# Performance work log

Measured on AMD Instinct MI355X. Metric: run time of the kernel, lower is better.

## Reference

```python
import jax, jax.numpy as jnp
import numpy as np

BITS = 4
SPLIT_BITS = 4  # `ratio` arg plays the role of split_bits in the torch Function


def _chunk_quant(src, bits):
    """src: [n_chunks, chunk_elems...]; quantize each chunk with its own min/max."""
    reduce_axes = tuple(range(1, src.ndim))
    mn = src.min(axis=reduce_axes, keepdims=True)
    mx = src.max(axis=reduce_axes, keepdims=True)
    levels = jnp.asarray(2 ** bits - 1, src.dtype)
    step = (mx - mn) / levels
    safe_step = jnp.where(step == 0, jnp.ones_like(step), step)
    # torch: round((s-min)/step) - 2^(b-1); then (+2^(b-1))*step + min  ==  round(...)*step + min
    q = jnp.round((src - mn) / safe_step) * safe_step + mn
    # if min == max the chunk is passed through unchanged
    return jnp.where(mn == mx, src, q)


def setup_inputs() -> dict:
    key = jax.random.key(0)
    x = jax.random.normal(key, (16, 2048, 2048), dtype=jnp.float32)
    return {"x": x}


def reference(x) -> jnp.ndarray:
    shape = x.shape
    flat = x.reshape(-1)
    n_chunks = 2 ** SPLIT_BITS  # 16; flat.size divisible by 16 by construction
    order = jnp.argsort(flat)            # ascending sort permutation
    src = flat[order].reshape(n_chunks, -1)
    q = _chunk_quant(src, BITS).reshape(-1)
    # scatter quantized values back to original positions: out[order[i]] = q[i]
    inv = jnp.argsort(order)
    out = q[inv]
    return out.reshape(shape)
```

## Files before the change

### kernel.cpp

```cpp
#include <hip/hip_runtime.h>
#include <math.h>

#define L1BITS 14
#define L1B 16384
#define L1W (L1B / 2)
#define H1_BLOCKS 512
#define SLOTS 32
#define L2BITS 9
#define L2B 512
#define L3BITS 9
#define L3B 512
#define H2_BLOCKS 256
#define H2W (SLOTS * L2B / 2)

__device__ unsigned int g_part1[H1_BLOCKS * L1W];
__device__ unsigned int g_part2[H2_BLOCKS * H2W];
__device__ unsigned int g_hist1[L1B];
__device__ unsigned int g_coarse1[L1B / 256];
__device__ unsigned int g_hist2[SLOTS * L2B];
__device__ unsigned int g_hist3[SLOTS * L3B];
__device__ unsigned char g_sid1[L1B];
__device__ unsigned char g_sid2[SLOTS * L2B];

__device__ unsigned int g_bin1[32], g_res1[32];
__device__ int          g_slot1[32];
__device__ unsigned int g_bin2[32], g_res2[32];
__device__ int          g_slot2[32];
__device__ float        g_mn[16], g_mx[16];
__device__ unsigned int g_tkey[16];

__device__ __forceinline__ unsigned int f2key(float f) {
    unsigned int b = __float_as_uint(f);
    return (b & 0x80000000u) ? ~b : (b | 0x80000000u);
}
__device__ __forceinline__ float key2f(unsigned int k) {
    unsigned int b = (k & 0x80000000u) ? (k & 0x7FFFFFFFu) : ~k;
    return __uint_as_float(b);
}

__global__ void zero_scratch() {
    int i = blockIdx.x * blockDim.x + threadIdx.x;
    int stride = gridDim.x * blockDim.x;
    for (int j = i; j < L1B; j += stride) g_hist1[j] = 0u;
    for (int j = i; j < SLOTS * L2B; j += stride) g_hist2[j] = 0u;
    for (int j = i; j < SLOTS * L3B; j += stride) g_hist3[j] = 0u;
    unsigned int* s1 = (unsigned int*)g_sid1;
    for (int j = i; j < L1B / 4; j += stride) s1[j] = 0u;
    unsigned int* s2 = (unsigned int*)g_sid2;
    for (int j = i; j < SLOTS * L2B / 4; j += stride) s2[j] = 0u;
    if (i < L1B / 256) g_coarse1[i] = 0u;
}

__global__ void hist1_kernel(const float4* __restrict__ x, int n4) {
    __shared__ unsigned int h[2 * L1W];
    for (int j = threadIdx.x; j < 2 * L1W; j += blockDim.x) h[j] = 0u;
    __syncthreads();
    unsigned int* hp = &h[((threadIdx.x >> 6) & 1) * L1W];
    int stride = gridDim.x * blockDim.x;
    for (int i = blockIdx.x * blockDim.x + threadIdx.x; i < n4; i += stride) {
        float4 v = x[i];
        float vv[4] = {v.x, v.y, v.z, v.w};
#pragma unroll
        for (int k = 0; k < 4; ++k) {
            unsigned int b = f2key(vv[k]) >> (32 - L1BITS);
            atomicAdd(&hp[b >> 1], 1u << ((b & 1) << 4));
        }
    }
    __syncthreads();
    for (int j = threadIdx.x; j < L1W; j += blockDim.x) {
        unsigned int a = h[j], b = h[L1W + j];
        unsigned int lo = (a & 0xFFFFu) + (b & 0xFFFFu);
        unsigned int hi = (a >> 16) + (b >> 16);
        g_part1[blockIdx.x * L1W + j] = lo | (hi << 16);
    }
}

__global__ void reduce1_kernel() {
    int t = blockIdx.x * blockDim.x + threadIdx.x;
    int w = t & (L1W - 1);
    int chunk = t >> 13;
    const unsigned int* p = &g_part1[(chunk * 64) * L1W + w];
    unsigned int lo = 0, hi = 0;
#pragma unroll 8
    for (int b = 0; b < 64; ++b) {
        unsigned int u = p[b * L1W];
        lo += u & 0xFFFFu;
        hi += u >> 16;
    }
    atomicAdd(&g_hist1[2 * w], lo);
    atomicAdd(&g_hist1[2 * w + 1], hi);
    unsigned int s = lo + hi;
#pragma unroll
    for (int off = 32; off; off >>= 1) s += (unsigned int)__shfl_down((int)s, off, 64);
    if ((threadIdx.x & 63) == 0) atomicAdd(&g_coarse1[w >> 7], s);
}

__device__ __forceinline__ void wave_select(const unsigned int* __restrict__ hist,
                                            int nbins, unsigned int r,
                                            unsigned int* out_bin, unsigned int* out_res) {
    int lane = threadIdx.x & 63;
    unsigned int base = 0;
    for (int k = 0; k < nbins; k += 64) {
        unsigned int v = hist[k + lane];
        unsigned int incl = v;
#pragma unroll
        for (int off = 1; off < 64; off <<= 1) {
            unsigned int t = (unsigned int)__shfl_up((int)incl, off, 64);
            if (lane >= off) incl += t;
        }
        unsigned int total = (unsigned int)__shfl((int)incl, 63, 64);
        if (r < base + total) {
            unsigned long long m = __ballot(base + incl > r);
            int fl = __ffsll((long long)m) - 1;
            unsigned int incl_fl = (unsigned int)__shfl((int)incl, fl, 64);
            unsigned int v_fl = (unsigned int)__shfl((int)v, fl, 64);
            *out_bin = (unsigned int)(k + fl);
            *out_res = r - (base + incl_fl - v_fl);
            return;
        }
        base += total;
    }
    *out_bin = (unsigned int)(nbins - 1);
    *out_res = 0;
}

__global__ void select1_kernel(unsigned int n) {
    __shared__ unsigned int s_bin[32], s_res[32];
    int wid = threadIdx.x >> 6;
    unsigned int M = n >> 4;
    for (int i = wid; i < 32; i += 16) {
        unsigned int c = (unsigned int)(i >> 1);
        unsigned int r = (i & 1) ? ((c + 1) * M - 1u) : (c * M);
        unsigned int g, rg, b, res;
        wave_select(g_coarse1, L1B / 256, r, &g, &rg);
        wave_select(g_hist1 + (g << 8), 256, rg, &b, &res);
        if ((threadIdx.x & 63) == 0) { s_bin[i] = (g << 8) | b; s_res[i] = res; }
    }
    __syncthreads();
    if (threadIdx.x == 0) {
        int nu = 0;
        for (int i = 0; i < 32; ++i) {
            unsigned int b = s_bin[i];
            if (g_sid1[b] == 0) g_sid1[b] = (unsigned char)(++nu);
            g_slot1[i] = g_sid1[b] - 1;
            g_bin1[i] = b;
            g_res1[i] = s_res[i];
        }
    }
}

__global__ void hist2_kernel(const float4* __restrict__ x, int n4) {
    __shared__ unsigned int h2[H2W];
    __shared__ unsigned char sid1[L1B];
    for (int j = threadIdx.x; j < H2W; j += blockDim.x) h2[j] = 0u;
    unsigned int* s1w = (unsigned int*)sid1;
    for (int j = threadIdx.x; j < L1B / 4; j += blockDim.x) s1w[j] = ((const unsigned int*)g_sid1)[j];
    __syncthreads();
    int stride = gridDim.x * blockDim.x;
    for (int i = blockIdx.x * blockDim.x + threadIdx.x; i < n4; i += stride) {
        float4 v = x[i];
        float vv[4] = {v.x, v.y, v.z, v.w};
#pragma unroll
        for (int k = 0; k < 4; ++k) {
            unsigned int key = f2key(vv[k]);
            unsigned int s = sid1[key >> (32 - L1BITS)];
            if (s) {
                unsigned int c = ((s - 1) << L2BITS) | ((key >> L3BITS) & (L2B - 1));
                atomicAdd(&h2[c >> 1], 1u << ((c & 1) << 4));
            }
        }
    }
    __syncthreads();
    for (int j = threadIdx.x; j < H2W; j += blockDim.x)
        g_part2[blockIdx.x * H2W + j] = h2[j];
}

__global__ void reduce2_kernel() {
    int t = blockIdx.x * blockDim.x + threadIdx.x;
    int w = t & (H2W - 1);
    int chunk = t >> 13;
    const unsigned int* p = &g_part2[(chunk * 32) * H2W + w];
    unsigned int lo = 0, hi = 0;
#pragma unroll 8
    for (int b = 0; b < 32; ++b) {
        unsigned int u = p[b * H2W];
        lo += u & 0xFFFFu;
        hi += u >> 16;
    }
    atomicAdd(&g_hist2[2 * w], lo);
    atomicAdd(&g_hist2[2 * w + 1], hi);
}

__global__ void select2_kernel() {
    __shared__ unsigned int s_bin[32], s_res[32];
    int wid = threadIdx.x >> 6;
    for (int i = wid; i < 32; i += 16) {
        int s = g_slot1[i];
        unsigned int b, res;
        wave_select(g_hist2 + (s << L2BITS), L2B, g_res1[i], &b, &res);
        if ((threadIdx.x & 63) == 0) { s_bin[i] = b; s_res[i] = res; }
    }
    __syncthreads();
    if (threadIdx.x == 0) {
        int nu = 0;
        for (int i = 0; i < 32; ++i) {
            int p = g_slot1[i] * L2B + (int)s_bin[i];
            if (g_sid2[p] == 0) g_sid2[p] = (unsigned char)(++nu);
            g_slot2[i] = g_sid2[p] - 1;
            g_bin2[i] = s_bin[i];
            g_res2[i] = s_res[i];
        }
    }
}

__global__ void hist3_kernel(const float4* __restrict__ x, int n4) {
    __shared__ unsigned char sid1[L1B];
    __shared__ unsigned char sid2[SLOTS * L2B];
    unsigned int* s1w = (unsigned int*)sid1;
    for (int j = threadIdx.x; j < L1B / 4; j += blockDim.x) s1w[j] = ((const unsigned int*)g_sid1)[j];
    unsigned int* s2w = (unsigned int*)sid2;
    for (int j = threadIdx.x; j < SLOTS * L2B / 4; j += blockDim.x) s2w[j] = ((const unsigned int*)g_sid2)[j];
    __syncthreads();
    int stride = gridDim.x * blockDim.x;
    for (int i = blockIdx.x * blockDim.x + threadIdx.x; i < n4; i += stride) {
        float4 v = x[i];
        float vv[4] = {v.x, v.y, v.z, v.w};
#pragma unroll
        for (int k = 0; k < 4; ++k) {
            unsigned int key = f2key(vv[k]);
            unsigned int s = sid1[key >> (32 - L1BITS)];
            if (s) {
                unsigned int s2 = sid2[((s - 1) << L2BITS) | ((key >> L3BITS) & (L2B - 1))];
                if (s2) atomicAdd(&g_hist3[((s2 - 1) << L3BITS) | (key & (L3B - 1))], 1u);
            }
        }
    }
}

__global__ void select3_kernel() {
    __shared__ unsigned int s_key[32];
    int wid = threadIdx.x >> 6;
    for (int i = wid; i < 32; i += 16) {
        int s2 = g_slot2[i];
        unsigned int b, res;
        wave_select(g_hist3 + (s2 << L3BITS), L3B, g_res2[i], &b, &res);
        if ((threadIdx.x & 63) == 0)
            s_key[i] = (g_bin1[i] << (32 - L1BITS)) | (g_bin2[i] << L3BITS) | b;
    }
    __syncthreads();
    if (threadIdx.x < 16) {
        int c = threadIdx.x;
        unsigned int klo = s_key[2 * c];
        unsigned int khi = s_key[2 * c + 1];
        g_mn[c] = key2f(klo);
        g_mx[c] = key2f(khi);
        g_tkey[c] = (c == 0) ? 0u : klo;
    }
}

__global__ void quant_kernel(const float4* __restrict__ x, float4* __restrict__ out, int n4) {
    __shared__ float s_mn[16], s_mx[16];
    __shared__ unsigned int s_t[16];
    if (threadIdx.x < 16) {
        s_mn[threadIdx.x] = g_mn[threadIdx.x];
        s_mx[threadIdx.x] = g_mx[threadIdx.x];
        s_t[threadIdx.x]  = g_tkey[threadIdx.x];
    }
    __syncthreads();
    int stride = gridDim.x * blockDim.x;
    for (int i = blockIdx.x * blockDim.x + threadIdx.x; i < n4; i += stride) {
        float4 v = x[i];
        float r[4] = {v.x, v.y, v.z, v.w};
#pragma unroll
        for (int k = 0; k < 4; ++k) {
            float xv = r[k];
            unsigned int key = f2key(xv);
            int c = (key >= s_t[8]) ? 8 : 0;
            if (key >= s_t[c + 4]) c += 4;
            if (key >= s_t[c + 2]) c += 2;
            if (key >= s_t[c + 1]) c += 1;
            float mn = s_mn[c], mx = s_mx[c];
            float outv;
            if (mn == mx) {
                outv = xv;
            } else {
                float st = (mx - mn) / 15.0f;
                if (st == 0.0f) st = 1.0f;
                float q = rintf((xv - mn) / st);
                outv = __fadd_rn(__fmul_rn(q, st), mn);
            }
            r[k] = outv;
        }
        out[i] = make_float4(r[0], r[1], r[2], r[3]);
    }
}

extern "C" void kernel_launch(void* const* d_in, const int* in_sizes, int n_in,
                              void* d_out, int out_size, void* d_ws, size_t ws_size,
                              hipStream_t stream) {
    const float* x = (const float*)d_in[0];
    float* out = (float*)d_out;
    int n  = in_sizes[0];
    int n4 = n / 4;

    zero_scratch<<<64, 256, 0, stream>>>();
    hist1_kernel<<<H1_BLOCKS, 512, 0, stream>>>((const float4*)x, n4);
    reduce1_kernel<<<256, 256, 0, stream>>>();
    select1_kernel<<<1, 1024, 0, stream>>>((unsigned int)n);
    hist2_kernel<<<H2_BLOCKS, 512, 0, stream>>>((const float4*)x, n4);
    reduce2_kernel<<<256, 256, 0, stream>>>();
    select2_kernel<<<1, 1024, 0, stream>>>();
    hist3_kernel<<<1024, 512, 0, stream>>>((const float4*)x, n4);
    select3_kernel<<<1, 1024, 0, stream>>>();
    quant_kernel<<<4096, 256, 0, stream>>>((const float4*)x, (float4*)out, n4);
}
```

Baseline: 707.2 us.

## Compact candidate keys during level-2 pass to skip third full input scan

The level-2 histogram pass now also writes the keys that fall in selected level-1 bins into per-block segments, and the level-3 histogram reads only those compacted keys instead of rescanning the whole input. This removes one full read of the 256 MB tensor and the separate reduce2 kernel, since level-2 partials are atomically merged straight into the global histogram. Zeroing of scratch moves into hist1, hist1 drops its duplicated shared histogram and runs with larger blocks, and the loops are unrolled to batch loads. The cost is extra global writes for candidate keys, wave-level ballot/atomic overhead, and a fixed segment size that silently truncates if too many keys are selected.

```diff
diff --git a/kernel.cpp b/kernel.cpp
--- a/kernel.cpp
+++ b/kernel.cpp
@@ -10,11 +10,13 @@
 #define L2B 512
 #define L3BITS 9
 #define L3B 512
-#define H2_BLOCKS 256
 #define H2W (SLOTS * L2B / 2)
+#define CBLK 256
+#define SEGSZ 262144
 
 __device__ unsigned int g_part1[H1_BLOCKS * L1W];
-__device__ unsigned int g_part2[H2_BLOCKS * H2W];
+__device__ unsigned int g_keys[CBLK * SEGSZ];
+__device__ unsigned int g_kcnt[CBLK];
 __device__ unsigned int g_hist1[L1B];
 __device__ unsigned int g_coarse1[L1B / 256];
 __device__ unsigned int g_hist2[SLOTS * L2B];
@@ -38,41 +40,42 @@
     return __uint_as_float(b);
 }
 
-__global__ void zero_scratch() {
-    int i = blockIdx.x * blockDim.x + threadIdx.x;
+__global__ void hist1_kernel(const float4* __restrict__ x, int n4) {
+    int gtid = blockIdx.x * blockDim.x + threadIdx.x;
+    if (gtid < L1B) g_hist1[gtid] = 0u;
+    if (gtid < SLOTS * L2B) g_hist2[gtid] = 0u;
+    if (gtid < SLOTS * L3B) g_hist3[gtid] = 0u;
+    if (gtid < L1B / 4) ((unsigned int*)g_sid1)[gtid] = 0u;
+    if (gtid < SLOTS * L2B / 4) ((unsigned int*)g_sid2)[gtid] = 0u;
+    if (gtid < L1B / 256) g_coarse1[gtid] = 0u;
+
+    __shared__ unsigned int h[L1W];
+    for (int j = threadIdx.x; j < L1W; j += blockDim.x) h[j] = 0u;
+    __syncthreads();
     int stride = gridDim.x * blockDim.x;
-    for (int j = i; j < L1B; j += stride) g_hist1[j] = 0u;
-    for (int j = i; j < SLOTS * L2B; j += stride) g_hist2[j] = 0u;
-    for (int j = i; j < SLOTS * L3B; j += stride) g_hist3[j] = 0u;
-    unsigned int* s1 = (unsigned int*)g_sid1;
-    for (int j = i; j < L1B / 4; j += stride) s1[j] = 0u;
-    unsigned int* s2 = (unsigned int*)g_sid2;
-    for (int j = i; j < SLOTS * L2B / 4; j += stride) s2[j] = 0u;
-    if (i < L1B / 256) g_coarse1[i] = 0u;
-}
-
-__global__ void hist1_kernel(const float4* __restrict__ x, int n4) {
-    __shared__ unsigned int h[2 * L1W];
-    for (int j = threadIdx.x; j < 2 * L1W; j += blockDim.x) h[j] = 0u;
-    __syncthreads();
-    unsigned int* hp = &h[((threadIdx.x >> 6) & 1) * L1W];
-    int stride = gridDim.x * blockDim.x;
-    for (int i = blockIdx.x * blockDim.x + threadIdx.x; i < n4; i += stride) {
+    int i = gtid;
+    for (; i + 3 * stride < n4; i += 4 * stride) {
+        float4 a = x[i], b = x[i + stride], c = x[i + 2 * stride], d = x[i + 3 * stride];
+        float vv[16] = {a.x, a.y, a.z, a.w, b.x, b.y, b.z, b.w,
+                        c.x, c.y, c.z, c.w, d.x, d.y, d.z, d.w};
+#pragma unroll
+        for (int k = 0; k < 16; ++k) {
+            unsigned int bn = f2key(vv[k]) >> (32 - L1BITS);
+            atomicAdd(&h[bn >> 1], 1u << ((bn & 1) << 4));
+        }
+    }
+    for (; i < n4; i += stride) {
         float4 v = x[i];
         float vv[4] = {v.x, v.y, v.z, v.w};
 #pragma unroll
         for (int k = 0; k < 4; ++k) {
-            unsigned int b = f2key(vv[k]) >> (32 - L1BITS);
-            atomicAdd(&hp[b >> 1], 1u << ((b & 1) << 4));
-        }
-    }
-    __syncthreads();
-    for (int j = threadIdx.x; j < L1W; j += blockDim.x) {
-        unsigned int a = h[j], b = h[L1W + j];
-        unsigned int lo = (a & 0xFFFFu) + (b & 0xFFFFu);
-        unsigned int hi = (a >> 16) + (b >> 16);
-        g_part1[blockIdx.x * L1W + j] = lo | (hi << 16);
-    }
+            unsigned int bn = f2key(vv[k]) >> (32 - L1BITS);
+            atomicAdd(&h[bn >> 1], 1u << ((bn & 1) << 4));
+        }
+    }
+    __syncthreads();
+    for (int j = threadIdx.x; j < L1W; j += blockDim.x)
+        g_part1[blockIdx.x * L1W + j] = h[j];
 }
 
 __global__ void reduce1_kernel() {
@@ -149,46 +152,65 @@
     }
 }
 
-__global__ void hist2_kernel(const float4* __restrict__ x, int n4) {
+__device__ __forceinline__ void compact_one(unsigned int key,
+                                            const unsigned char* sid1,
+                                            unsigned int* h2, unsigned int* s_cnt,
+                                            unsigned int segbase) {
+    unsigned int s = sid1[key >> (32 - L1BITS)];
+    bool sel = (s != 0);
+    unsigned int word = ((s - 1) << 18) | (key & 0x3FFFFu);
+    unsigned long long m = __ballot(sel);
+    if (m) {
+        int lane = threadIdx.x & 63;
+        int leader = __ffsll((long long)m) - 1;
+        unsigned int base = 0;
+        if (lane == leader) base = atomicAdd(s_cnt, (unsigned int)__popcll(m));
+        base = (unsigned int)__shfl((int)base, leader, 64);
+        if (sel) {
+            unsigned int off = (unsigned int)__popcll(m & ((1ull << lane) - 1ull));
+            unsigned int p = base + off;
+            if (p < SEGSZ) g_keys[segbase + p] = word;
+            unsigned int c = word >> 9;
+            atomicAdd(&h2[c >> 1], 1u << ((c & 1) << 4));
+        }
+    }
+}
+
+__global__ void compact2_kernel(const float4* __restrict__ x, int n4) {
     __shared__ unsigned int h2[H2W];
     __shared__ unsigned char sid1[L1B];
+    __shared__ unsigned int s_cnt;
     for (int j = threadIdx.x; j < H2W; j += blockDim.x) h2[j] = 0u;
     unsigned int* s1w = (unsigned int*)sid1;
     for (int j = threadIdx.x; j < L1B / 4; j += blockDim.x) s1w[j] = ((const unsigned int*)g_sid1)[j];
-    __syncthreads();
+    if (threadIdx.x == 0) s_cnt = 0u;
+    __syncthreads();
+    unsigned int segbase = blockIdx.x * SEGSZ;
     int stride = gridDim.x * blockDim.x;
-    for (int i = blockIdx.x * blockDim.x + threadIdx.x; i < n4; i += stride) {
+    int i = blockIdx.x * blockDim.x + threadIdx.x;
+    for (; i + 3 * stride < n4; i += 4 * stride) {
+        float4 a = x[i], b = x[i + stride], c = x[i + 2 * stride], d = x[i + 3 * stride];
+        float vv[16] = {a.x, a.y, a.z, a.w, b.x, b.y, b.z, b.w,
+                        c.x, c.y, c.z, c.w, d.x, d.y, d.z, d.w};
+#pragma unroll
+        for (int k = 0; k < 16; ++k) compact_one(f2key(vv[k]), sid1, h2, &s_cnt, segbase);
+    }
+    for (; i < n4; i += stride) {
         float4 v = x[i];
         float vv[4] = {v.x, v.y, v.z, v.w};
 #pragma unroll
-        for (int k = 0; k < 4; ++k) {
-            unsigned int key = f2key(vv[k]);
-            unsigned int s = sid1[key >> (32 - L1BITS)];
-            if (s) {
-                unsigned int c = ((s - 1) << L2BITS) | ((key >> L3BITS) & (L2B - 1));
-                atomicAdd(&h2[c >> 1], 1u << ((c & 1) << 4));
-            }
-        }
-    }
-    __syncthreads();
-    for (int j = threadIdx.x; j < H2W; j += blockDim.x)
-        g_part2[blockIdx.x * H2W + j] = h2[j];
-}
-
-__global__ void reduce2_kernel() {
-    int t = blockIdx.x * blockDim.x + threadIdx.x;
-    int w = t & (H2W - 1);
-    int chunk = t >> 13;
-    const unsigned int* p = &g_part2[(chunk * 32) * H2W + w];
-    unsigned int lo = 0, hi = 0;
-#pragma unroll 8
-    for (int b = 0; b < 32; ++b) {
-        unsigned int u = p[b * H2W];
-        lo += u & 0xFFFFu;
-        hi += u >> 16;
-    }
-    atomicAdd(&g_hist2[2 * w], lo);
-    atomicAdd(&g_hist2[2 * w + 1], hi);
+        for (int k = 0; k < 4; ++k) compact_one(f2key(vv[k]), sid1, h2, &s_cnt, segbase);
+    }
+    __syncthreads();
+    if (threadIdx.x == 0) g_kcnt[blockIdx.x] = s_cnt;
+    for (int j = threadIdx.x; j < H2W; j += blockDim.x) {
+        unsigned int u = h2[j];
+        if (u) {
+            unsigned int lo = u & 0xFFFFu, hi = u >> 16;
+            if (lo) atomicAdd(&g_hist2[2 * j], lo);
+            if (hi) atomicAdd(&g_hist2[2 * j + 1], hi);
+        }
+    }
 }
 
 __global__ void select2_kernel() {
@@ -213,27 +235,17 @@
     }
 }
 
-__global__ void hist3_kernel(const float4* __restrict__ x, int n4) {
-    __shared__ unsigned char sid1[L1B];
+__global__ void hist3c_kernel() {
     __shared__ unsigned char sid2[SLOTS * L2B];
-    unsigned int* s1w = (unsigned int*)sid1;
-    for (int j = threadIdx.x; j < L1B / 4; j += blockDim.x) s1w[j] = ((const unsigned int*)g_sid1)[j];
     unsigned int* s2w = (unsigned int*)sid2;
     for (int j = threadIdx.x; j < SLOTS * L2B / 4; j += blockDim.x) s2w[j] = ((const unsigned int*)g_sid2)[j];
     __syncthreads();
-    int stride = gridDim.x * blockDim.x;
-    for (int i = blockIdx.x * blockDim.x + threadIdx.x; i < n4; i += stride) {
-        float4 v = x[i];
-        float vv[4] = {v.x, v.y, v.z, v.w};
-#pragma unroll
-        for (int k = 0; k < 4; ++k) {
-            unsigned int key = f2key(vv[k]);
-            unsigned int s = sid1[key >> (32 - L1BITS)];
-            if (s) {
-                unsigned int s2 = sid2[((s - 1) << L2BITS) | ((key >> L3BITS) & (L2B - 1))];
-                if (s2) atomicAdd(&g_hist3[((s2 - 1) << L3BITS) | (key & (L3B - 1))], 1u);
-            }
-        }
+    unsigned int cnt = g_kcnt[blockIdx.x];
+    const unsigned int* seg = &g_keys[blockIdx.x * SEGSZ];
+    for (unsigned int i = threadIdx.x; i < cnt; i += blockDim.x) {
+        unsigned int w = seg[i];
+        unsigned int s2 = sid2[w >> 9];
+        if (s2) atomicAdd(&g_hist3[((s2 - 1) << L3BITS) | (w & (L3B - 1))], 1u);
     }
 }
 
@@ -258,6 +270,21 @@
     }
 }
 
+__device__ __forceinline__ float quant_one(float xv, const float* s_mn, const float* s_mx,
+                                           const unsigned int* s_t) {
+    unsigned int key = f2key(xv);
+    int c = (key >= s_t[8]) ? 8 : 0;
+    if (key >= s_t[c + 4]) c += 4;
+    if (key >= s_t[c + 2]) c += 2;
+    if (key >= s_t[c + 1]) c += 1;
+    float mn = s_mn[c], mx = s_mx[c];
+    if (mn == mx) return xv;
+    float st = (mx - mn) / 15.0f;
+    if (st == 0.0f) st = 1.0f;
+    float q = rintf((xv - mn) / st);
+    return __fadd_rn(__fmul_rn(q, st), mn);
+}
+
 __global__ void quant_kernel(const float4* __restrict__ x, float4* __restrict__ out, int n4) {
     __shared__ float s_mn[16], s_mx[16];
     __shared__ unsigned int s_t[16];
@@ -268,30 +295,23 @@
     }
     __syncthreads();
     int stride = gridDim.x * blockDim.x;
-    for (int i = blockIdx.x * blockDim.x + threadIdx.x; i < n4; i += stride) {
+    int i = blockIdx.x * blockDim.x + threadIdx.x;
+    for (; i + stride < n4; i += 2 * stride) {
+        float4 a = x[i], b = x[i + stride];
+        float4 oa, ob;
+        oa.x = quant_one(a.x, s_mn, s_mx, s_t); oa.y = quant_one(a.y, s_mn, s_mx, s_t);
+        oa.z = quant_one(a.z, s_mn, s_mx, s_t); oa.w = quant_one(a.w, s_mn, s_mx, s_t);
+        ob.x = quant_one(b.x, s_mn, s_mx, s_t); ob.y = quant_one(b.y, s_mn, s_mx, s_t);
+        ob.z = quant_one(b.z, s_mn, s_mx, s_t); ob.w = quant_one(b.w, s_mn, s_mx, s_t);
+        out[i] = oa;
+        out[i + stride] = ob;
+    }
+    for (; i < n4; i += stride) {
         float4 v = x[i];
-        float r[4] = {v.x, v.y, v.z, v.w};
-#pragma unroll
-        for (int k = 0; k < 4; ++k) {
-            float xv = r[k];
-            unsigned int key = f2key(xv);
-            int c = (key >= s_t[8]) ? 8 : 0;
-            if (key >= s_t[c + 4]) c += 4;
-            if (key >= s_t[c + 2]) c += 2;
-            if (key >= s_t[c + 1]) c += 1;
-            float mn = s_mn[c], mx = s_mx[c];
-            float outv;
-            if (mn == mx) {
-                outv = xv;
-            } else {
-                float st = (mx - mn) / 15.0f;
-                if (st == 0.0f) st = 1.0f;
-                float q = rintf((xv - mn) / st);
-                outv = __fadd_rn(__fmul_rn(q, st), mn);
-            }
-            r[k] = outv;
-        }
-        out[i] = make_float4(r[0], r[1], r[2], r[3]);
+        float4 o;
+        o.x = quant_one(v.x, s_mn, s_mx, s_t); o.y = quant_one(v.y, s_mn, s_mx, s_t);
+        o.z = quant_one(v.z, s_mn, s_mx, s_t); o.w = quant_one(v.w, s_mn, s_mx, s_t);
+        out[i] = o;
     }
 }
 
@@ -303,14 +323,12 @@
     int n  = in_sizes[0];
     int n4 = n / 4;
 
-    zero_scratch<<<64, 256, 0, stream>>>();
-    hist1_kernel<<<H1_BLOCKS, 512, 0, stream>>>((const float4*)x, n4);
+    hist1_kernel<<<H1_BLOCKS, 1024, 0, stream>>>((const float4*)x, n4);
     reduce1_kernel<<<256, 256, 0, stream>>>();
     select1_kernel<<<1, 1024, 0, stream>>>((unsigned int)n);
-    hist2_kernel<<<H2_BLOCKS, 512, 0, stream>>>((const float4*)x, n4);
-    reduce2_kernel<<<256, 256, 0, stream>>>();
+    compact2_kernel<<<CBLK, 512, 0, stream>>>((const float4*)x, n4);
     select2_kernel<<<1, 1024, 0, stream>>>();
-    hist3_kernel<<<1024, 512, 0, stream>>>((const float4*)x, n4);
+    hist3c_kernel<<<CBLK, 512, 0, stream>>>();
     select3_kernel<<<1, 1024, 0, stream>>>();
     quant_kernel<<<4096, 256, 0, stream>>>((const float4*)x, (float4*)out, n4);
 }
```

Measured after the change: 720.9 us. About the same (+1.9%).
